# Optimization experiments

Hardware: AMD Instinct MI355X
Metric: run time of the kernel (lower is better)

## Reference

```python
import jax, jax.numpy as jnp
import numpy as np

C_IN, C_OUT, KH, KW = 64, 128, 3, 3
STRIDE, PAD, DIL = 1, 1, 1
EPS = 1e-5


def setup_inputs() -> dict:
    key = jax.random.key(0)
    ks = jax.random.split(key, 7)
    B, H, W = 8, 112, 112
    x = jax.random.normal(ks[0], (B, C_IN, H, W), dtype=jnp.float32)
    # offset conv: produces 2*KH*KW offset channels; small init keeps offsets sane
    w_off = jax.random.normal(ks[1], (2 * KH * KW, C_IN, KH, KW), dtype=jnp.float32) * 0.01
    b_off = jax.random.normal(ks[2], (2 * KH * KW,), dtype=jnp.float32) * 0.01
    # deformable conv weight/bias
    fan_in = C_IN * KH * KW
    w_dcn = jax.random.normal(ks[3], (C_OUT, C_IN, KH, KW), dtype=jnp.float32) / np.sqrt(fan_in)
    b_dcn = jax.random.normal(ks[4], (C_OUT,), dtype=jnp.float32) * 0.01
    gamma = jnp.ones((C_OUT,), dtype=jnp.float32)
    beta = jnp.zeros((C_OUT,), dtype=jnp.float32)
    return {"x": x, "w_off": w_off, "b_off": b_off, "w_dcn": w_dcn,
            "b_dcn": b_dcn, "gamma": gamma, "beta": beta}


def _conv2d(x, w, b):
    y = jax.lax.conv_general_dilated(
        x, w, window_strides=(STRIDE, STRIDE),
        padding=((PAD, PAD), (PAD, PAD)),
        rhs_dilation=(DIL, DIL),
        dimension_numbers=("NCHW", "OIHW", "NCHW"))
    return y + b[None, :, None, None]


def _deform_conv(x, offset, w, b):
    # x: [B,C,H,W]; offset: [B, 2*KH*KW, Ho, Wo] with (dy, dx) pairs per tap
    B, C, H, W = x.shape
    KK = KH * KW
    Ho, Wo = offset.shape[2], offset.shape[3]
    off = offset.reshape(B, KK, 2, Ho, Wo)
    ky = (jnp.arange(KK) // KW).astype(jnp.float32)  # kernel row per tap
    kx = (jnp.arange(KK) % KW).astype(jnp.float32)
    base_y = (jnp.arange(Ho) * STRIDE - PAD).astype(jnp.float32)
    base_x = (jnp.arange(Wo) * STRIDE - PAD).astype(jnp.float32)
    # sampling positions [B, KK, Ho, Wo]
    py = off[:, :, 0] + base_y[None, None, :, None] + (ky * DIL)[None, :, None, None]
    px = off[:, :, 1] + base_x[None, None, None, :] + (kx * DIL)[None, :, None, None]

    y0 = jnp.floor(py)
    x0 = jnp.floor(px)
    wy1 = py - y0  # weight for y0+1
    wx1 = px - x0
    y0i = y0.astype(jnp.int32)
    x0i = x0.astype(jnp.int32)

    x_flat = x.reshape(B, C, H * W)

    def gather_corner(yi, xi, wgt):
        # yi, xi, wgt: [B, KK, Ho, Wo]
        valid = (yi >= 0) & (yi < H) & (xi >= 0) & (xi < W)
        idx = jnp.clip(yi, 0, H - 1) * W + jnp.clip(xi, 0, W - 1)
        idx = idx.reshape(B, -1)  # [B, KK*Ho*Wo]
        vals = jnp.take_along_axis(x_flat, idx[:, None, :], axis=2)  # [B, C, N]
        coef = (wgt * valid.astype(wgt.dtype)).reshape(B, 1, -1)
        return vals * coef

    samp = (gather_corner(y0i,     x0i,     (1 - wy1) * (1 - wx1))
            + gather_corner(y0i,     x0i + 1, (1 - wy1) * wx1)
            + gather_corner(y0i + 1, x0i,     wy1 * (1 - wx1))
            + gather_corner(y0i + 1, x0i + 1, wy1 * wx1))
    samp = samp.reshape(B, C, KK, Ho, Wo)
    out = jnp.einsum("bckhw,ock->bohw", samp, w.reshape(w.shape[0], C, KK))
    return out + b[None, :, None, None]


def reference(x, w_off, b_off, w_dcn, b_dcn, gamma, beta):
    offset = _conv2d(x, w_off, b_off)
    y = _deform_conv(x, offset, w_dcn, b_dcn)
    # BatchNorm2d (training mode: biased batch stats) + ReLU
    mean = jnp.mean(y, axis=(0, 2, 3))
    var = jnp.var(y, axis=(0, 2, 3))
    yhat = (y - mean[None, :, None, None]) * jax.lax.rsqrt(var + EPS)[None, :, None, None]
    y = gamma[None, :, None, None] * yhat + beta[None, :, None, None]
    return jax.nn.relu(y)
```

## Files before the change

kernel.cpp:

```cpp
#include <hip/hip_runtime.h>

#define H    112
#define W    112
#define HW   12544
#define CIN  64
#define COUT 128
#define BATCH 8
#define KK   9
#define OFFC 18
#define EPS  1e-5f
#define TP   32
#define KDIM 576
#define KPAD 584

typedef unsigned short ushort;
typedef unsigned int uint;
typedef __attribute__((ext_vector_type(8))) short short8;
typedef __attribute__((ext_vector_type(8))) ushort ushort8;
typedef __attribute__((ext_vector_type(4))) float floatx4;

__device__ __forceinline__ ushort f2bf(float f) {
  uint u = __float_as_uint(f);
  u = (u + 0x7FFFu + ((u >> 16) & 1u)) >> 16;
  return (ushort)u;
}

__global__ __launch_bounds__(256) void k_transpose_x(
    const float* __restrict__ x, float* __restrict__ xT) {
  __shared__ float tile[64][65];
  int b = blockIdx.y;
  int p0 = blockIdx.x * 64;
  int tid = threadIdx.x;
  int j = tid & 63, cb = tid >> 6;
#pragma unroll
  for (int i = 0; i < 16; ++i) {
    int ci = cb * 16 + i;
    tile[ci][j] = x[((size_t)(b * CIN + ci)) * HW + p0 + j];
  }
  __syncthreads();
  int ci2 = tid & 63;
#pragma unroll
  for (int i = 0; i < 16; ++i) {
    int p = cb * 16 + i;
    xT[((size_t)b * HW + p0 + p) * 64 + ci2] = tile[ci2][p];
  }
}

__global__ __launch_bounds__(256) void k_prep_w(
    const float* __restrict__ w_off, const float* __restrict__ w_dcn,
    float* __restrict__ w_r, ushort* __restrict__ w_mf) {
  int i = blockIdx.x * 256 + threadIdx.x;
  if (i < OFFC * KDIM) {
    int oc = i / KDIM, rem = i - oc * KDIM;
    int ci = rem / KK, kk = rem - ci * KK;
    w_r[(kk * 64 + ci) * OFFC + oc] = w_off[i];
  } else if (i < OFFC * KDIM + COUT * KDIM) {
    int jj = i - OFFC * KDIM;
    int co = jj / KDIM, rem = jj - co * KDIM;
    int ci = rem / KK, kk = rem - ci * KK;
    w_mf[co * KDIM + kk * 64 + ci] = f2bf(w_dcn[jj]);
  }
}

__global__ __launch_bounds__(256) void k_offset_conv(
    const float* __restrict__ xT, const float* __restrict__ w_r,
    const float* __restrict__ bias, float* __restrict__ out) {
  int b = blockIdx.y;
  int p = blockIdx.x * 256 + threadIdx.x;
  int ho = p / W, wo = p - ho * W;
  float acc[OFFC];
#pragma unroll
  for (int oc = 0; oc < OFFC; ++oc) acc[oc] = bias[oc];
  const float* xb = xT + (size_t)b * HW * 64;
  for (int t = 0; t < 9; ++t) {
    int yy = ho + t / 3 - 1;
    int xx = wo + t % 3 - 1;
    bool valid = (yy >= 0) & (yy < H) & (xx >= 0) & (xx < W);
    const float4* src = (const float4*)(xb + ((size_t)(yy * W + xx) << 6));
    const float* wbase = w_r + t * 64 * OFFC;
    if (valid) {
#pragma unroll 2
      for (int cig = 0; cig < 16; ++cig) {
        float4 v = src[cig];
#pragma unroll
        for (int jj = 0; jj < 4; ++jj) {
          float xv = (jj == 0) ? v.x : (jj == 1) ? v.y : (jj == 2) ? v.z : v.w;
          const float* wp = wbase + (cig * 4 + jj) * OFFC;
#pragma unroll
          for (int oc = 0; oc < OFFC; ++oc)
            acc[oc] = fmaf(xv, wp[oc], acc[oc]);
        }
      }
    }
  }
#pragma unroll
  for (int oc = 0; oc < OFFC; ++oc)
    out[((size_t)b * OFFC + oc) * HW + p] = acc[oc];
}

__global__ __launch_bounds__(256) void k_deform(
    const float* __restrict__ xT, const float* __restrict__ off,
    const ushort* __restrict__ w_mf, float* __restrict__ y) {
  __shared__ float4 s_w[KK][TP];
  __shared__ int4   s_i[KK][TP];
  __shared__ ushort samp[TP][KPAD];

  int b = blockIdx.y;
  int p0 = blockIdx.x * TP;
  int tid = threadIdx.x;
  const float* xb = xT + (size_t)b * HW * 64;

  for (int it = tid; it < KK * TP; it += 256) {
    int kk = it >> 5;
    int px = it & 31;
    int p = p0 + px;
    int ho = p / W, wo = p - ho * W;
    float dy = off[((size_t)b * OFFC + 2 * kk) * HW + p];
    float dx = off[((size_t)b * OFFC + 2 * kk + 1) * HW + p];
    float py = dy + (float)(ho - 1 + kk / 3);
    float pxx = dx + (float)(wo - 1 + kk % 3);
    float y0f = floorf(py), x0f = floorf(pxx);
    float wy1 = py - y0f, wx1 = pxx - x0f;
    int y0 = (int)y0f, x0 = (int)x0f;
    int y1 = y0 + 1, x1 = x0 + 1;
    float vy0 = (y0 >= 0 && y0 < H) ? 1.f : 0.f;
    float vy1 = (y1 >= 0 && y1 < H) ? 1.f : 0.f;
    float vx0 = (x0 >= 0 && x0 < W) ? 1.f : 0.f;
    float vx1 = (x1 >= 0 && x1 < W) ? 1.f : 0.f;
    int cy0 = min(max(y0, 0), H - 1), cy1 = min(max(y1, 0), H - 1);
    int cx0 = min(max(x0, 0), W - 1), cx1 = min(max(x1, 0), W - 1);
    s_w[kk][px] = make_float4((1.f - wy1) * (1.f - wx1) * vy0 * vx0,
                              (1.f - wy1) * wx1 * vy0 * vx1,
                              wy1 * (1.f - wx1) * vy1 * vx0,
                              wy1 * wx1 * vy1 * vx1);
    s_i[kk][px] = make_int4((cy0 * W + cx0) << 6, (cy0 * W + cx1) << 6,
                            (cy1 * W + cx0) << 6, (cy1 * W + cx1) << 6);
  }
  __syncthreads();

#pragma unroll
  for (int r = 0; r < 9; ++r) {
    int it = tid + r * 256;
    int px = it / 72;
    int rem = it - px * 72;
    int kk = rem >> 3;
    int cig = rem & 7;
    int ci0 = cig * 8;
    float4 wv = s_w[kk][px];
    int4 iv = s_i[kk][px];
    const float4* c0 = (const float4*)(xb + iv.x + ci0);
    const float4* c1 = (const float4*)(xb + iv.y + ci0);
    const float4* c2 = (const float4*)(xb + iv.z + ci0);
    const float4* c3 = (const float4*)(xb + iv.w + ci0);
    float4 a0 = c0[0], a1 = c0[1];
    float4 b0 = c1[0], b1 = c1[1];
    float4 d0 = c2[0], d1 = c2[1];
    float4 e0 = c3[0], e1 = c3[1];
    float r0x = wv.x * a0.x + wv.y * b0.x + wv.z * d0.x + wv.w * e0.x;
    float r0y = wv.x * a0.y + wv.y * b0.y + wv.z * d0.y + wv.w * e0.y;
    float r0z = wv.x * a0.z + wv.y * b0.z + wv.z * d0.z + wv.w * e0.z;
    float r0w = wv.x * a0.w + wv.y * b0.w + wv.z * d0.w + wv.w * e0.w;
    float r1x = wv.x * a1.x + wv.y * b1.x + wv.z * d1.x + wv.w * e1.x;
    float r1y = wv.x * a1.y + wv.y * b1.y + wv.z * d1.y + wv.w * e1.y;
    float r1z = wv.x * a1.z + wv.y * b1.z + wv.z * d1.z + wv.w * e1.z;
    float r1w = wv.x * a1.w + wv.y * b1.w + wv.z * d1.w + wv.w * e1.w;
    ushort8 pk;
    pk[0] = f2bf(r0x); pk[1] = f2bf(r0y); pk[2] = f2bf(r0z); pk[3] = f2bf(r0w);
    pk[4] = f2bf(r1x); pk[5] = f2bf(r1y); pk[6] = f2bf(r1z); pk[7] = f2bf(r1w);
    *(ushort8*)&samp[px][kk * 64 + ci0] = pk;
  }
  __syncthreads();

  int wave = tid >> 6, lane = tid & 63;
  int row16 = lane & 15, quad = lane >> 4;
  int koff = quad * 8;
  int co_base = wave * 32;
  const short8* wa0 = (const short8*)(w_mf + (size_t)(co_base + row16) * KDIM + koff);
  const short8* wa1 = (const short8*)(w_mf + (size_t)(co_base + 16 + row16) * KDIM + koff);
  const short8* sb0 = (const short8*)&samp[row16][koff];
  const short8* sb1 = (const short8*)&samp[16 + row16][koff];

  floatx4 acc00 = {0.f, 0.f, 0.f, 0.f}, acc01 = acc00, acc10 = acc00, acc11 = acc00;
#pragma unroll
  for (int ks = 0; ks < KDIM / 32; ++ks) {
    short8 A0 = wa0[ks * 4];
    short8 A1 = wa1[ks * 4];
    short8 B0 = sb0[ks * 4 + 0 * 0];
    short8 B1 = sb1[ks * 4];
    B0 = *(const short8*)((const ushort*)&samp[row16][koff] + ks * 32);
    B1 = *(const short8*)((const ushort*)&samp[16 + row16][koff] + ks * 32);
    acc00 = __builtin_amdgcn_mfma_f32_16x16x32_bf16(A0, B0, acc00, 0, 0, 0);
    acc01 = __builtin_amdgcn_mfma_f32_16x16x32_bf16(A0, B1, acc01, 0, 0, 0);
    acc10 = __builtin_amdgcn_mfma_f32_16x16x32_bf16(A1, B0, acc10, 0, 0, 0);
    acc11 = __builtin_amdgcn_mfma_f32_16x16x32_bf16(A1, B1, acc11, 0, 0, 0);
  }

  float* yb = y + (size_t)b * COUT * HW + p0;
#pragma unroll
  for (int reg = 0; reg < 4; ++reg) {
    int r0 = quad * 4 + reg;
    yb[(size_t)(co_base + r0) * HW + row16]      = acc00[reg];
    yb[(size_t)(co_base + r0) * HW + 16 + row16] = acc01[reg];
    yb[(size_t)(co_base + 16 + r0) * HW + row16]      = acc10[reg];
    yb[(size_t)(co_base + 16 + r0) * HW + 16 + row16] = acc11[reg];
  }
}

__global__ __launch_bounds__(256) void k_stats(const float* __restrict__ y,
                                               float* __restrict__ stats) {
  int c = blockIdx.x & 127;
  int half = blockIdx.x >> 7;
  int tid = threadIdx.x;
  float s = 0.f, s2 = 0.f;
#pragma unroll
  for (int bb = 0; bb < 2; ++bb) {
    int b = half * 2 + bb;
    const float4* yp = (const float4*)(y + ((size_t)b * COUT + c) * HW);
    for (int p = tid; p < HW / 4; p += 256) {
      float4 v = yp[p];
      s += v.x + v.y + v.z + v.w;
      s2 += v.x * v.x + v.y * v.y + v.z * v.z + v.w * v.w;
    }
  }
#pragma unroll
  for (int o = 32; o > 0; o >>= 1) {
    s += __shfl_down(s, o, 64);
    s2 += __shfl_down(s2, o, 64);
  }
  __shared__ float ls[4], ls2[4];
  int lane = tid & 63, wid = tid >> 6;
  if (lane == 0) { ls[wid] = s; ls2[wid] = s2; }
  __syncthreads();
  if (tid == 0) {
    atomicAdd(&stats[c], ls[0] + ls[1] + ls[2] + ls[3]);
    atomicAdd(&stats[COUT + c], ls2[0] + ls2[1] + ls2[2] + ls2[3]);
  }
}

__global__ __launch_bounds__(256) void k_norm(const float* __restrict__ y,
                                              const float* __restrict__ stats,
                                              const float* __restrict__ gamma,
                                              const float* __restrict__ beta,
                                              float* __restrict__ out) {
  int i4 = blockIdx.x * 256 + threadIdx.x;
  const int total4 = BATCH * COUT * HW / 4;
  if (i4 >= total4) return;
  size_t i = (size_t)i4 * 4;
  int c = (int)((i / HW) & (COUT - 1));
  const float N = (float)(BATCH * HW);
  float m = stats[c] / N;
  float var = stats[COUT + c] / N - m * m;
  float r = rsqrtf(var + EPS);
  float g = gamma[c], bt = beta[c];
  float4 v = *(const float4*)&y[i];
  v.x = fmaxf(0.f, (v.x - m) * r * g + bt);
  v.y = fmaxf(0.f, (v.y - m) * r * g + bt);
  v.z = fmaxf(0.f, (v.z - m) * r * g + bt);
  v.w = fmaxf(0.f, (v.w - m) * r * g + bt);
  *(float4*)&out[i] = v;
}

extern "C" void kernel_launch(void* const* d_in, const int* in_sizes, int n_in,
                              void* d_out, int out_size, void* d_ws, size_t ws_size,
                              hipStream_t stream) {
  const float* x     = (const float*)d_in[0];
  const float* w_off = (const float*)d_in[1];
  const float* b_off = (const float*)d_in[2];
  const float* w_dcn = (const float*)d_in[3];
  const float* gamma = (const float*)d_in[5];
  const float* beta  = (const float*)d_in[6];
  float* out = (float*)d_out;

  float* ws = (float*)d_ws;
  float*  xT      = ws;
  float*  off_buf = xT + 6422528;
  float*  w_r     = off_buf + 1806336;
  ushort* w_mf    = (ushort*)(w_r + 10368);
  float*  y       = w_r + 10368 + 36864;
  float*  stats   = y + 12845056;

  hipMemsetAsync(stats, 0, 256 * sizeof(float), stream);
  k_transpose_x<<<dim3(HW / 64, BATCH), 256, 0, stream>>>(x, xT);
  k_prep_w<<<(OFFC * KDIM + COUT * KDIM + 255) / 256, 256, 0, stream>>>(w_off, w_dcn, w_r, w_mf);
  k_offset_conv<<<dim3(HW / 256, BATCH), 256, 0, stream>>>(xT, w_r, b_off, off_buf);
  k_deform<<<dim3(HW / TP, BATCH), 256, 0, stream>>>(xT, off_buf, w_mf, y);
  k_stats<<<512, 256, 0, stream>>>(y, stats);
  k_norm<<<(BATCH * COUT * HW / 4 + 255) / 256, 256, 0, stream>>>(y, stats, gamma, beta, out);
}
```

Before: 269.5 us.

## Fuse BN stats into deform kernel, split offset conv channels, widen deform blocks

Batch-norm sum and sum-of-squares are now computed from the MFMA accumulators inside the deform kernel with shuffles and atomics, which removes the separate stats pass that re-read the full output tensor. The offset conv splits the input channels across two waves per pixel and combines the halves through shared memory, so twice as many blocks run. The deform kernel moves to 512 threads with narrower gather work per thread and 16 output channels per wave. bf16 packing now uses a cheaper round-half-up with a perm instruction. Costs are more atomics on the stats buffer and slightly different bf16 rounding.

```diff
diff --git a/kernel.cpp b/kernel.cpp
--- a/kernel.cpp
+++ b/kernel.cpp
@@ -16,13 +16,18 @@
 typedef unsigned short ushort;
 typedef unsigned int uint;
 typedef __attribute__((ext_vector_type(8))) short short8;
-typedef __attribute__((ext_vector_type(8))) ushort ushort8;
 typedef __attribute__((ext_vector_type(4))) float floatx4;
 
 __device__ __forceinline__ ushort f2bf(float f) {
   uint u = __float_as_uint(f);
   u = (u + 0x7FFFu + ((u >> 16) & 1u)) >> 16;
   return (ushort)u;
+}
+
+__device__ __forceinline__ uint pack_bf2(float f0, float f1) {
+  uint u0 = __float_as_uint(f0) + 0x8000u;
+  uint u1 = __float_as_uint(f1) + 0x8000u;
+  return __builtin_amdgcn_perm(u1, u0, 0x07060302u);
 }
 
 __global__ __launch_bounds__(256) void k_transpose_x(
@@ -65,27 +70,32 @@
 __global__ __launch_bounds__(256) void k_offset_conv(
     const float* __restrict__ xT, const float* __restrict__ w_r,
     const float* __restrict__ bias, float* __restrict__ out) {
+  __shared__ float red[2][64][OFFC + 1];
   int b = blockIdx.y;
-  int p = blockIdx.x * 256 + threadIdx.x;
+  int tid = threadIdx.x;
+  int wave = tid >> 6, lane = tid & 63;
+  int cih = wave & 1;
+  int pair = wave >> 1;
+  int p = blockIdx.x * 128 + pair * 64 + lane;
   int ho = p / W, wo = p - ho * W;
   float acc[OFFC];
 #pragma unroll
-  for (int oc = 0; oc < OFFC; ++oc) acc[oc] = bias[oc];
-  const float* xb = xT + (size_t)b * HW * 64;
+  for (int oc = 0; oc < OFFC; ++oc) acc[oc] = 0.f;
+  const float* xb = xT + (size_t)b * HW * 64 + cih * 32;
   for (int t = 0; t < 9; ++t) {
     int yy = ho + t / 3 - 1;
     int xx = wo + t % 3 - 1;
     bool valid = (yy >= 0) & (yy < H) & (xx >= 0) & (xx < W);
     const float4* src = (const float4*)(xb + ((size_t)(yy * W + xx) << 6));
-    const float* wbase = w_r + t * 64 * OFFC;
+    const float* wbase = w_r + (t * 64 + cih * 32) * OFFC;
     if (valid) {
 #pragma unroll 2
-      for (int cig = 0; cig < 16; ++cig) {
-        float4 v = src[cig];
+      for (int cg = 0; cg < 8; ++cg) {
+        float4 v = src[cg];
 #pragma unroll
         for (int jj = 0; jj < 4; ++jj) {
           float xv = (jj == 0) ? v.x : (jj == 1) ? v.y : (jj == 2) ? v.z : v.w;
-          const float* wp = wbase + (cig * 4 + jj) * OFFC;
+          const float* wp = wbase + (cg * 4 + jj) * OFFC;
 #pragma unroll
           for (int oc = 0; oc < OFFC; ++oc)
             acc[oc] = fmaf(xv, wp[oc], acc[oc]);
@@ -93,14 +103,24 @@
       }
     }
   }
-#pragma unroll
-  for (int oc = 0; oc < OFFC; ++oc)
-    out[((size_t)b * OFFC + oc) * HW + p] = acc[oc];
-}
-
-__global__ __launch_bounds__(256) void k_deform(
+  if (cih) {
+#pragma unroll
+    for (int oc = 0; oc < OFFC; ++oc) red[pair][lane][oc] = acc[oc];
+  }
+  __syncthreads();
+  if (!cih) {
+#pragma unroll
+    for (int oc = 0; oc < OFFC; ++oc) {
+      float v = acc[oc] + red[pair][lane][oc] + bias[oc];
+      out[((size_t)b * OFFC + oc) * HW + p] = v;
+    }
+  }
+}
+
+__global__ __launch_bounds__(512) void k_deform(
     const float* __restrict__ xT, const float* __restrict__ off,
-    const ushort* __restrict__ w_mf, float* __restrict__ y) {
+    const ushort* __restrict__ w_mf, float* __restrict__ y,
+    float* __restrict__ stats) {
   __shared__ float4 s_w[KK][TP];
   __shared__ int4   s_i[KK][TP];
   __shared__ ushort samp[TP][KPAD];
@@ -110,9 +130,9 @@
   int tid = threadIdx.x;
   const float* xb = xT + (size_t)b * HW * 64;
 
-  for (int it = tid; it < KK * TP; it += 256) {
-    int kk = it >> 5;
-    int px = it & 31;
+  if (tid < KK * TP) {
+    int kk = tid >> 5;
+    int px = tid & 31;
     int p = p0 + px;
     int ho = p / W, wo = p - ho * W;
     float dy = off[((size_t)b * OFFC + 2 * kk) * HW + p];
@@ -140,100 +160,67 @@
 
 #pragma unroll
   for (int r = 0; r < 9; ++r) {
-    int it = tid + r * 256;
-    int px = it / 72;
-    int rem = it - px * 72;
-    int kk = rem >> 3;
-    int cig = rem & 7;
-    int ci0 = cig * 8;
+    int it = tid + r * 512;
+    int px = it / 144;
+    int rem = it - px * 144;
+    int kk = rem >> 4;
+    int cig = rem & 15;
+    int ci0 = cig * 4;
     float4 wv = s_w[kk][px];
     int4 iv = s_i[kk][px];
-    const float4* c0 = (const float4*)(xb + iv.x + ci0);
-    const float4* c1 = (const float4*)(xb + iv.y + ci0);
-    const float4* c2 = (const float4*)(xb + iv.z + ci0);
-    const float4* c3 = (const float4*)(xb + iv.w + ci0);
-    float4 a0 = c0[0], a1 = c0[1];
-    float4 b0 = c1[0], b1 = c1[1];
-    float4 d0 = c2[0], d1 = c2[1];
-    float4 e0 = c3[0], e1 = c3[1];
-    float r0x = wv.x * a0.x + wv.y * b0.x + wv.z * d0.x + wv.w * e0.x;
-    float r0y = wv.x * a0.y + wv.y * b0.y + wv.z * d0.y + wv.w * e0.y;
-    float r0z = wv.x * a0.z + wv.y * b0.z + wv.z * d0.z + wv.w * e0.z;
-    float r0w = wv.x * a0.w + wv.y * b0.w + wv.z * d0.w + wv.w * e0.w;
-    float r1x = wv.x * a1.x + wv.y * b1.x + wv.z * d1.x + wv.w * e1.x;
-    float r1y = wv.x * a1.y + wv.y * b1.y + wv.z * d1.y + wv.w * e1.y;
-    float r1z = wv.x * a1.z + wv.y * b1.z + wv.z * d1.z + wv.w * e1.z;
-    float r1w = wv.x * a1.w + wv.y * b1.w + wv.z * d1.w + wv.w * e1.w;
-    ushort8 pk;
-    pk[0] = f2bf(r0x); pk[1] = f2bf(r0y); pk[2] = f2bf(r0z); pk[3] = f2bf(r0w);
-    pk[4] = f2bf(r1x); pk[5] = f2bf(r1y); pk[6] = f2bf(r1z); pk[7] = f2bf(r1w);
-    *(ushort8*)&samp[px][kk * 64 + ci0] = pk;
+    float4 c0 = *(const float4*)(xb + iv.x + ci0);
+    float4 c1 = *(const float4*)(xb + iv.y + ci0);
+    float4 c2 = *(const float4*)(xb + iv.z + ci0);
+    float4 c3 = *(const float4*)(xb + iv.w + ci0);
+    float r0 = wv.x * c0.x + wv.y * c1.x + wv.z * c2.x + wv.w * c3.x;
+    float r1 = wv.x * c0.y + wv.y * c1.y + wv.z * c2.y + wv.w * c3.y;
+    float r2 = wv.x * c0.z + wv.y * c1.z + wv.z * c2.z + wv.w * c3.z;
+    float r3 = wv.x * c0.w + wv.y * c1.w + wv.z * c2.w + wv.w * c3.w;
+    uint2 pk = make_uint2(pack_bf2(r0, r1), pack_bf2(r2, r3));
+    *(uint2*)&samp[px][kk * 64 + ci0] = pk;
   }
   __syncthreads();
 
   int wave = tid >> 6, lane = tid & 63;
   int row16 = lane & 15, quad = lane >> 4;
   int koff = quad * 8;
-  int co_base = wave * 32;
-  const short8* wa0 = (const short8*)(w_mf + (size_t)(co_base + row16) * KDIM + koff);
-  const short8* wa1 = (const short8*)(w_mf + (size_t)(co_base + 16 + row16) * KDIM + koff);
-  const short8* sb0 = (const short8*)&samp[row16][koff];
-  const short8* sb1 = (const short8*)&samp[16 + row16][koff];
-
-  floatx4 acc00 = {0.f, 0.f, 0.f, 0.f}, acc01 = acc00, acc10 = acc00, acc11 = acc00;
+  int co_base = wave * 16;
+  const ushort* wa = w_mf + (size_t)(co_base + row16) * KDIM + koff;
+  const ushort* sb0 = &samp[row16][koff];
+  const ushort* sb1 = &samp[16 + row16][koff];
+
+  floatx4 acc0 = {0.f, 0.f, 0.f, 0.f}, acc1 = acc0;
 #pragma unroll
   for (int ks = 0; ks < KDIM / 32; ++ks) {
-    short8 A0 = wa0[ks * 4];
-    short8 A1 = wa1[ks * 4];
-    short8 B0 = sb0[ks * 4 + 0 * 0];
-    short8 B1 = sb1[ks * 4];
-    B0 = *(const short8*)((const ushort*)&samp[row16][koff] + ks * 32);
-    B1 = *(const short8*)((const ushort*)&samp[16 + row16][koff] + ks * 32);
-    acc00 = __builtin_amdgcn_mfma_f32_16x16x32_bf16(A0, B0, acc00, 0, 0, 0);
-    acc01 = __builtin_amdgcn_mfma_f32_16x16x32_bf16(A0, B1, acc01, 0, 0, 0);
-    acc10 = __builtin_amdgcn_mfma_f32_16x16x32_bf16(A1, B0, acc10, 0, 0, 0);
-    acc11 = __builtin_amdgcn_mfma_f32_16x16x32_bf16(A1, B1, acc11, 0, 0, 0);
+    short8 A  = *(const short8*)(wa + ks * 32);
+    short8 B0 = *(const short8*)(sb0 + ks * 32);
+    short8 B1 = *(const short8*)(sb1 + ks * 32);
+    acc0 = __builtin_amdgcn_mfma_f32_16x16x32_bf16(A, B0, acc0, 0, 0, 0);
+    acc1 = __builtin_amdgcn_mfma_f32_16x16x32_bf16(A, B1, acc1, 0, 0, 0);
   }
 
   float* yb = y + (size_t)b * COUT * HW + p0;
 #pragma unroll
   for (int reg = 0; reg < 4; ++reg) {
     int r0 = quad * 4 + reg;
-    yb[(size_t)(co_base + r0) * HW + row16]      = acc00[reg];
-    yb[(size_t)(co_base + r0) * HW + 16 + row16] = acc01[reg];
-    yb[(size_t)(co_base + 16 + r0) * HW + row16]      = acc10[reg];
-    yb[(size_t)(co_base + 16 + r0) * HW + 16 + row16] = acc11[reg];
-  }
-}
-
-__global__ __launch_bounds__(256) void k_stats(const float* __restrict__ y,
-                                               float* __restrict__ stats) {
-  int c = blockIdx.x & 127;
-  int half = blockIdx.x >> 7;
-  int tid = threadIdx.x;
-  float s = 0.f, s2 = 0.f;
-#pragma unroll
-  for (int bb = 0; bb < 2; ++bb) {
-    int b = half * 2 + bb;
-    const float4* yp = (const float4*)(y + ((size_t)b * COUT + c) * HW);
-    for (int p = tid; p < HW / 4; p += 256) {
-      float4 v = yp[p];
-      s += v.x + v.y + v.z + v.w;
-      s2 += v.x * v.x + v.y * v.y + v.z * v.z + v.w * v.w;
-    }
-  }
-#pragma unroll
-  for (int o = 32; o > 0; o >>= 1) {
-    s += __shfl_down(s, o, 64);
-    s2 += __shfl_down(s2, o, 64);
-  }
-  __shared__ float ls[4], ls2[4];
-  int lane = tid & 63, wid = tid >> 6;
-  if (lane == 0) { ls[wid] = s; ls2[wid] = s2; }
-  __syncthreads();
-  if (tid == 0) {
-    atomicAdd(&stats[c], ls[0] + ls[1] + ls[2] + ls[3]);
-    atomicAdd(&stats[COUT + c], ls2[0] + ls2[1] + ls2[2] + ls2[3]);
+    yb[(size_t)(co_base + r0) * HW + row16]      = acc0[reg];
+    yb[(size_t)(co_base + r0) * HW + 16 + row16] = acc1[reg];
+  }
+
+#pragma unroll
+  for (int reg = 0; reg < 4; ++reg) {
+    float s = acc0[reg] + acc1[reg];
+    float q = acc0[reg] * acc0[reg] + acc1[reg] * acc1[reg];
+#pragma unroll
+    for (int m = 1; m < 16; m <<= 1) {
+      s += __shfl_xor(s, m, 64);
+      q += __shfl_xor(q, m, 64);
+    }
+    if (row16 == 0) {
+      int co = co_base + quad * 4 + reg;
+      atomicAdd(&stats[co], s);
+      atomicAdd(&stats[COUT + co], q);
+    }
   }
 }
 
@@ -282,8 +269,7 @@
   hipMemsetAsync(stats, 0, 256 * sizeof(float), stream);
   k_transpose_x<<<dim3(HW / 64, BATCH), 256, 0, stream>>>(x, xT);
   k_prep_w<<<(OFFC * KDIM + COUT * KDIM + 255) / 256, 256, 0, stream>>>(w_off, w_dcn, w_r, w_mf);
-  k_offset_conv<<<dim3(HW / 256, BATCH), 256, 0, stream>>>(xT, w_r, b_off, off_buf);
-  k_deform<<<dim3(HW / TP, BATCH), 256, 0, stream>>>(xT, off_buf, w_mf, y);
-  k_stats<<<512, 256, 0, stream>>>(y, stats);
+  k_offset_conv<<<dim3(HW / 128, BATCH), 256, 0, stream>>>(xT, w_r, b_off, off_buf);
+  k_deform<<<dim3(HW / TP, BATCH), 512, 0, stream>>>(xT, off_buf, w_mf, y, stats);
   k_norm<<<(BATCH * COUT * HW / 4 + 255) / 256, 256, 0, stream>>>(y, stats, gamma, beta, out);
 }
```

Result: slower. 612.0 us (+127.1%).
